# Optimization experiments

Hardware: AMD Instinct MI355X
Metric: run time of the kernel (lower is better)

## Reference

```python
import jax, jax.numpy as jnp
import numpy as np

N_NODES = 100000
N_EDGES = 1600000
N_GRAPHS = 256
NEG_SLOPE_GAT = 0.2   # GATConv default
NEG_SLOPE_ACT = 0.01  # F.leaky_relu default


def _leaky(x, s):
    return jnp.where(x >= 0, x, s * x)


def _gat_layer(x, src, dst, W, a_src, a_dst, b, n):
    # h = W x ; per-node attention logits
    h = x @ W                      # [N, D]
    al_s = h @ a_src               # [N]
    al_d = h @ a_dst               # [N]
    e = _leaky(al_s[src] + al_d[dst], NEG_SLOPE_GAT)  # [E]
    # segment softmax over incoming edges of each dst node
    m = jax.ops.segment_max(e, dst, num_segments=n)
    m = jnp.where(jnp.isfinite(m), m, 0.0)
    ex = jnp.exp(e - m[dst])
    s = jax.ops.segment_sum(ex, dst, num_segments=n)
    alpha = ex / (s[dst] + 1e-16)
    out = jax.ops.segment_sum(h[src] * alpha[:, None], dst, num_segments=n)
    return out + b


def setup_inputs() -> dict:
    key = jax.random.key(0)
    ks = jax.random.split(key, 12)
    x = jax.random.normal(ks[0], (N_NODES, 72), dtype=jnp.float32)
    edge_index = jax.random.randint(ks[1], (2, N_EDGES), 0, N_NODES, dtype=jnp.int64)
    batch = jnp.sort(jax.random.randint(ks[2], (N_NODES,), 0, N_GRAPHS, dtype=jnp.int64))
    def glorot(k, shape):
        fan = shape[0] + shape[-1]
        return jax.random.normal(k, shape, dtype=jnp.float32) * jnp.sqrt(2.0 / fan)
    return {
        "x": x, "edge_index": edge_index, "batch": batch,
        "W1": glorot(ks[3], (72, 64)),
        "a_src1": glorot(ks[4], (64,)), "a_dst1": glorot(ks[5], (64,)),
        "b1": jnp.zeros((64,), jnp.float32),
        "W2": glorot(ks[6], (64, 64)),
        "a_src2": glorot(ks[7], (64,)), "a_dst2": glorot(ks[8], (64,)),
        "b2": jnp.zeros((64,), jnp.float32),
        "fcW": glorot(ks[9], (64, 2)),
        "fcb": jnp.zeros((2,), jnp.float32),
    }


def reference(x, edge_index, batch, W1, a_src1, a_dst1, b1, W2, a_src2, a_dst2, b2, fcW, fcb):
    n = x.shape[0]
    # PyG GATConv adds self-loops by default
    loops = jnp.arange(n, dtype=edge_index.dtype)
    src = jnp.concatenate([edge_index[0], loops])
    dst = jnp.concatenate([edge_index[1], loops])
    h = _gat_layer(x, src, dst, W1, a_src1, a_dst1, b1, n)
    h = _leaky(h, NEG_SLOPE_ACT)
    h = _gat_layer(h, src, dst, W2, a_src2, a_dst2, b2, n)
    # global mean pool over graphs
    sums = jax.ops.segment_sum(h, batch, num_segments=N_GRAPHS)
    cnt = jax.ops.segment_sum(jnp.ones((n,), h.dtype), batch, num_segments=N_GRAPHS)
    pooled = sums / jnp.maximum(cnt, 1.0)[:, None]
    # dropout is identity at inference
    return pooled @ fcW + fcb
```

## Files before the change

### kernel.cpp

```cpp
#include <hip/hip_runtime.h>
#include <hip/hip_bf16.h>
#include <math.h>


#define NPB 256
#define EPB 4096
#define PSTRIDE 4608
#define XPAD 68

__device__ __forceinline__ unsigned int f2bf(float v) {
    unsigned int b = __float_as_uint(v);
    b += 0x7FFFu + ((b >> 16) & 1u);
    return b >> 16;
}

__device__ __forceinline__ int scanIncl256(int v, int t, int* wsum) {
    int lane = t & 63, wv = t >> 6;
#pragma unroll
    for (int o = 1; o < 64; o <<= 1) {
        int u = __shfl_up(v, o);
        if (lane >= o) v += u;
    }
    if (lane == 63) wsum[wv] = v;
    __syncthreads();
    int base = 0;
#pragma unroll
    for (int i = 0; i < 3; i++) base += (i < wv) ? wsum[i] : 0;
    __syncthreads();
    return v + base;
}

__global__ __launch_bounds__(256) void partition(const int* __restrict__ ei,
                                                 int E, int NB,
                                                 int* __restrict__ bcur,
                                                 unsigned int* __restrict__ pairs) {
    __shared__ int h[512];
    __shared__ int ls[512];
    __shared__ int lcur[512];
    __shared__ int hb[512];
    __shared__ int s2[256];
    __shared__ int wsum[4];
    __shared__ unsigned int Qp[EPB];
    __shared__ unsigned short Bq[EPB];
    int t = threadIdx.x;
    for (int i = t; i < 512; i += 256) h[i] = 0;
    __syncthreads();
    int i0 = blockIdx.x * EPB;
    unsigned int val[16];
    int bk[16];
    const int4* s4p = (const int4*)(ei);
    const int4* d4p = (const int4*)(ei + E);
#pragma unroll
    for (int k = 0; k < 4; k++) {
        int vbase = (i0 >> 2) + k * 256 + t;
        int i = vbase << 2;
        if (i < E) {
            int4 s4 = s4p[vbase];
            int4 d4 = d4p[vbase];
            int ss[4] = {s4.x, s4.y, s4.z, s4.w};
            int dd[4] = {d4.x, d4.y, d4.z, d4.w};
#pragma unroll
            for (int j = 0; j < 4; j++) {
                int e = k * 4 + j;
                bk[e] = dd[j] >> 8;
                val[e] = (unsigned)ss[j] | ((unsigned)(dd[j] & 255) << 24);
                atomicAdd(&h[bk[e]], 1);
            }
        } else {
#pragma unroll
            for (int j = 0; j < 4; j++) bk[k * 4 + j] = -1;
        }
    }
    __syncthreads();
    int p0 = h[2 * t], p1 = h[2 * t + 1];
    int incl = scanIncl256(p0 + p1, t, wsum);
    s2[t] = incl;
    int ex = incl - p0 - p1;
    ls[2 * t] = ex;           ls[2 * t + 1] = ex + p0;
    lcur[2 * t] = ex;         lcur[2 * t + 1] = ex + p0;
    __syncthreads();
    for (int b = t; b < NB; b += 256)
        hb[b] = h[b] ? atomicAdd(&bcur[b], h[b]) : 0;
    __syncthreads();
#pragma unroll
    for (int e = 0; e < 16; e++) {
        if (bk[e] < 0) continue;
        int pos = atomicAdd(&lcur[bk[e]], 1);
        Qp[pos] = val[e];
        Bq[pos] = (unsigned short)bk[e];
    }
    __syncthreads();
    int total = s2[255];
    for (int j = t; j < total; j += 256) {
        int bkj = Bq[j];
        int gp = hb[bkj] + (j - ls[bkj]);
        if (gp < PSTRIDE)
            pairs[(size_t)bkj * PSTRIDE + gp] = Qp[j];
    }
}

__global__ __launch_bounds__(256) void build_csr(const unsigned int* __restrict__ pairs,
                                                 const int* __restrict__ bcur,
                                                 int n, int NB,
                                                 int* __restrict__ rowptr,
                                                 int* __restrict__ srcs) {
    int b = blockIdx.x, t = threadIdx.x;
    __shared__ int c[512];
    __shared__ int s2[256];
    __shared__ int wsum[4];
    __shared__ int sbase, stot;
    __shared__ unsigned int Q[PSTRIDE];
    __shared__ int S[NPB + PSTRIDE];
    __shared__ int hist[256];
    __shared__ int hcur[256];
    int c0 = (2 * t < NB) ? min(bcur[2 * t], PSTRIDE) : 0;
    int c1 = (2 * t + 1 < NB) ? min(bcur[2 * t + 1], PSTRIDE) : 0;
    c[2 * t] = c0; c[2 * t + 1] = c1;
    hist[t] = 0;
    __syncthreads();
    int incl = scanIncl256(c0 + c1, t, wsum);
    s2[t] = incl;
    __syncthreads();
    if (t == 0) {
        int p = b >> 1;
        int ex = s2[p] - (c[2 * p] + c[2 * p + 1]);
        sbase = ex + ((b & 1) ? c[b & ~1] : 0);
        stot = s2[255];
    }
    __syncthreads();
    int d0 = b << 8;
    int nb = min(NPB, n - d0);
    int cnt_b = c[b];
    int csr0 = sbase + d0;
    const unsigned int* pb = pairs + (size_t)b * PSTRIDE;

    for (int j = t; j < cnt_b; j += 256)
        atomicAdd(&hist[(pb[j] & 0xFFFFFFu) >> 9], 1);
    __syncthreads();
    int hv = hist[t];
    int hincl = scanIncl256(hv, t, wsum);
    hcur[t] = hincl - hv;
    __syncthreads();
    for (int j = t; j < cnt_b; j += 256) {
        unsigned int p = pb[j];
        int pos = atomicAdd(&hcur[(p & 0xFFFFFFu) >> 9], 1);
        Q[pos] = p;
    }
    __syncthreads();

    __shared__ int deg[NPB];
    __shared__ int cur[NPB];
    deg[t] = (t < nb) ? 1 : 0;
    __syncthreads();
    for (int j = t; j < cnt_b; j += 256)
        atomicAdd(&deg[Q[j] >> 24], 1);
    __syncthreads();
    int v = deg[t];
    int dincl = scanIncl256(v, t, wsum);
    int excl = dincl - v;
    if (t < nb) {
        rowptr[d0 + t] = csr0 + excl;
        S[excl] = d0 + t;
        cur[t] = excl + 1;
    }
    __syncthreads();
    for (int j = t; j < cnt_b; j += 256) {
        unsigned int p = Q[j];
        int off = atomicAdd(&cur[p >> 24], 1);
        S[off] = (int)(p & 0x00FFFFFFu);
    }
    __syncthreads();
    int seg = nb + cnt_b;
    for (int j = t; j < seg; j += 256)
        srcs[csr0 + j] = S[j];
    if (b == 0 && t == 0) rowptr[n] = n + stot;
}

template <int IN_DIM>
__global__ __launch_bounds__(256) void node_gemm(const float* __restrict__ x,
                                                 const float* __restrict__ W,
                                                 const float* __restrict__ a_src,
                                                 const float* __restrict__ a_dst,
                                                 const float* __restrict__ bias_in,
                                                 float slope_in,
                                                 unsigned short* __restrict__ h16,
                                                 float* __restrict__ al_s,
                                                 float* __restrict__ al_d,
                                                 int n) {
    __shared__ float Ws[IN_DIM * 64];
    __shared__ float xs[IN_DIM][XPAD];
    int t = threadIdx.x;
    int nbase = blockIdx.x * 64;

    for (int idx = t; idx < IN_DIM * 16; idx += 256)
        ((float4*)Ws)[idx] = ((const float4*)W)[idx];
    const float* xb = x + (size_t)nbase * IN_DIM;
    int lim = min(64, n - nbase) * IN_DIM;
    constexpr int NV = (64 * IN_DIM) / 4;
    for (int idx = t; idx < NV; idx += 256) {
        int f0 = idx * 4;
        float4 v = make_float4(0.0f, 0.0f, 0.0f, 0.0f);
        if (f0 < lim) v = ((const float4*)xb)[idx];
        int node = f0 / IN_DIM;
        int k = f0 - node * IN_DIM;
        if (bias_in) {
            v.x += bias_in[k + 0];
            v.y += bias_in[k + 1];
            v.z += bias_in[k + 2];
            v.w += bias_in[k + 3];
            v.x = (v.x >= 0.0f) ? v.x : slope_in * v.x;
            v.y = (v.y >= 0.0f) ? v.y : slope_in * v.y;
            v.z = (v.z >= 0.0f) ? v.z : slope_in * v.z;
            v.w = (v.w >= 0.0f) ? v.w : slope_in * v.w;
        }
        xs[k + 0][node] = v.x;
        xs[k + 1][node] = v.y;
        xs[k + 2][node] = v.z;
        xs[k + 3][node] = v.w;
    }
    __syncthreads();

    int cg = t & 15;
    int ng = t >> 4;
    float acc[4][4] = {};
#pragma unroll 8
    for (int k = 0; k < IN_DIM; k++) {
        float4 xv = *(const float4*)&xs[k][ng * 4];
        float4 wv = *(const float4*)&Ws[k * 64 + cg * 4];
        float xa[4] = {xv.x, xv.y, xv.z, xv.w};
        float wa[4] = {wv.x, wv.y, wv.z, wv.w};
#pragma unroll
        for (int i = 0; i < 4; i++)
#pragma unroll
            for (int j = 0; j < 4; j++)
                acc[i][j] += xa[i] * wa[j];
    }

    float4 as4 = *(const float4*)(a_src + cg * 4);
    float4 ad4 = *(const float4*)(a_dst + cg * 4);
#pragma unroll
    for (int i = 0; i < 4; i++) {
        int node = nbase + ng * 4 + i;
        if (node < n) {
            uint2 p;
            p.x = f2bf(acc[i][0]) | (f2bf(acc[i][1]) << 16);
            p.y = f2bf(acc[i][2]) | (f2bf(acc[i][3]) << 16);
            *(uint2*)(h16 + (size_t)node * 64 + cg * 4) = p;
        }
        float vs = acc[i][0] * as4.x + acc[i][1] * as4.y +
                   acc[i][2] * as4.z + acc[i][3] * as4.w;
        float vd = acc[i][0] * ad4.x + acc[i][1] * ad4.y +
                   acc[i][2] * ad4.z + acc[i][3] * ad4.w;
#pragma unroll
        for (int o = 8; o; o >>= 1) {
            vs += __shfl_xor(vs, o);
            vd += __shfl_xor(vd, o);
        }
        if (cg == 0 && node < n) { al_s[node] = vs; al_d[node] = vd; }
    }
}

__device__ __forceinline__ void bf8_fma(float* acc, uint4 q, float w) {
    acc[0] += w * __uint_as_float(q.x << 16);
    acc[1] += w * __uint_as_float(q.x & 0xFFFF0000u);
    acc[2] += w * __uint_as_float(q.y << 16);
    acc[3] += w * __uint_as_float(q.y & 0xFFFF0000u);
    acc[4] += w * __uint_as_float(q.z << 16);
    acc[5] += w * __uint_as_float(q.z & 0xFFFF0000u);
    acc[6] += w * __uint_as_float(q.w << 16);
    acc[7] += w * __uint_as_float(q.w & 0xFFFF0000u);
}

__global__ __launch_bounds__(256) void gat_aggregate(const int* __restrict__ rowptr,
                                                     const int* __restrict__ srcs,
                                                     const float* __restrict__ als,
                                                     const float* __restrict__ ald,
                                                     const unsigned short* __restrict__ h16,
                                                     float* __restrict__ hout,
                                                     int n) {
    int t = threadIdx.x;
    int sub = t >> 3, lane = t & 7;
    int node = blockIdx.x * 32 + sub;
    if (node >= n) return;
    int beg = rowptr[node], end = rowptr[node + 1];
    float aldv = ald[node];
    const unsigned short* hb = h16 + lane * 8;

    float acc[8] = {};
    float sm = 0.0f;
    int j = beg;
    if (j + 4 <= end) {
        int s0 = srcs[j], s1 = srcs[j + 1], s2 = srcs[j + 2], s3 = srcs[j + 3];
        for (; j + 8 <= end; j += 4) {
            int n0 = srcs[j + 4], n1 = srcs[j + 5];
            int n2 = srcs[j + 6], n3 = srcs[j + 7];
            float e0 = als[s0] + aldv, e1 = als[s1] + aldv;
            float e2 = als[s2] + aldv, e3 = als[s3] + aldv;
            uint4 q0 = *(const uint4*)(hb + (size_t)s0 * 64);
            uint4 q1 = *(const uint4*)(hb + (size_t)s1 * 64);
            uint4 q2 = *(const uint4*)(hb + (size_t)s2 * 64);
            uint4 q3 = *(const uint4*)(hb + (size_t)s3 * 64);
            e0 = (e0 >= 0.0f) ? e0 : 0.2f * e0;
            e1 = (e1 >= 0.0f) ? e1 : 0.2f * e1;
            e2 = (e2 >= 0.0f) ? e2 : 0.2f * e2;
            e3 = (e3 >= 0.0f) ? e3 : 0.2f * e3;
            float w0 = __expf(e0), w1 = __expf(e1);
            float w2 = __expf(e2), w3 = __expf(e3);
            sm += (w0 + w1) + (w2 + w3);
            bf8_fma(acc, q0, w0);
            bf8_fma(acc, q1, w1);
            bf8_fma(acc, q2, w2);
            bf8_fma(acc, q3, w3);
            s0 = n0; s1 = n1; s2 = n2; s3 = n3;
        }
        {
            float e0 = als[s0] + aldv, e1 = als[s1] + aldv;
            float e2 = als[s2] + aldv, e3 = als[s3] + aldv;
            uint4 q0 = *(const uint4*)(hb + (size_t)s0 * 64);
            uint4 q1 = *(const uint4*)(hb + (size_t)s1 * 64);
            uint4 q2 = *(const uint4*)(hb + (size_t)s2 * 64);
            uint4 q3 = *(const uint4*)(hb + (size_t)s3 * 64);
            e0 = (e0 >= 0.0f) ? e0 : 0.2f * e0;
            e1 = (e1 >= 0.0f) ? e1 : 0.2f * e1;
            e2 = (e2 >= 0.0f) ? e2 : 0.2f * e2;
            e3 = (e3 >= 0.0f) ? e3 : 0.2f * e3;
            float w0 = __expf(e0), w1 = __expf(e1);
            float w2 = __expf(e2), w3 = __expf(e3);
            sm += (w0 + w1) + (w2 + w3);
            bf8_fma(acc, q0, w0);
            bf8_fma(acc, q1, w1);
            bf8_fma(acc, q2, w2);
            bf8_fma(acc, q3, w3);
            j += 4;
        }
    }
    for (; j < end; j++) {
        int s = srcs[j];
        float e = als[s] + aldv;
        e = (e >= 0.0f) ? e : 0.2f * e;
        float w = __expf(e);
        uint4 q = *(const uint4*)(hb + (size_t)s * 64);
        sm += w;
        bf8_fma(acc, q, w);
    }

    float inv = 1.0f / (sm + 1e-16f);
    float4 o0 = make_float4(acc[0] * inv, acc[1] * inv, acc[2] * inv, acc[3] * inv);
    float4 o1 = make_float4(acc[4] * inv, acc[5] * inv, acc[6] * inv, acc[7] * inv);
    float* op = hout + (size_t)node * 64 + lane * 8;
    *(float4*)op = o0;
    *(float4*)(op + 4) = o1;
}

__global__ __launch_bounds__(256) void pool_fc(const float* __restrict__ hout,
                                               const float* __restrict__ b2,
                                               const int* __restrict__ batch,
                                               const float* __restrict__ fcW,
                                               const float* __restrict__ fcb,
                                               float* __restrict__ out, int n) {
    int g = blockIdx.x;
    int t = threadIdx.x;
    __shared__ int sLo, sHi;
    __shared__ float red[16][64];
    if (t == 0) {
        int lo = 0, hi = n;
        while (lo < hi) { int m = (lo + hi) >> 1; if (batch[m] < g) lo = m + 1; else hi = m; }
        sLo = lo;
    } else if (t == 64) {
        int lo = 0, hi = n;
        while (lo < hi) { int m = (lo + hi) >> 1; if (batch[m] < g + 1) lo = m + 1; else hi = m; }
        sHi = lo;
    }
    __syncthreads();
    int lo = sLo, hi = sHi;
    int q = t & 15;
    int r = t >> 4;
    float4 a4 = make_float4(0.0f, 0.0f, 0.0f, 0.0f);
    for (int node = lo + r; node < hi; node += 16) {
        float4 v = *(const float4*)(hout + (size_t)node * 64 + q * 4);
        a4.x += v.x; a4.y += v.y; a4.z += v.z; a4.w += v.w;
    }
    *(float4*)&red[r][q * 4] = a4;
    __syncthreads();
    if (t < 64) {
        float c = (float)(hi - lo);
        float s = 0.0f;
#pragma unroll
        for (int i = 0; i < 16; i++) s += red[i][t];
        s += c * b2[t];
        float cd = (c > 1.0f) ? c : 1.0f;
        float p = s / cd;
        float s0 = p * fcW[t * 2 + 0];
        float s1 = p * fcW[t * 2 + 1];
#pragma unroll
        for (int o = 32; o; o >>= 1) {
            s0 += __shfl_xor(s0, o);
            s1 += __shfl_xor(s1, o);
        }
        if (t == 0) {
            out[g * 2 + 0] = s0 + fcb[0];
            out[g * 2 + 1] = s1 + fcb[1];
        }
    }
}

extern "C" void kernel_launch(void* const* d_in, const int* in_sizes, int n_in,
                              void* d_out, int out_size, void* d_ws, size_t ws_size,
                              hipStream_t stream) {
    const float* x    = (const float*)d_in[0];
    const int*   ei   = (const int*)d_in[1];
    const int*   batch= (const int*)d_in[2];
    const float* W1   = (const float*)d_in[3];
    const float* as1  = (const float*)d_in[4];
    const float* ad1  = (const float*)d_in[5];
    const float* b1   = (const float*)d_in[6];
    const float* W2   = (const float*)d_in[7];
    const float* as2  = (const float*)d_in[8];
    const float* ad2  = (const float*)d_in[9];
    const float* b2   = (const float*)d_in[10];
    const float* fcW  = (const float*)d_in[11];
    const float* fcb  = (const float*)d_in[12];
    float* out = (float*)d_out;

    const int N = in_sizes[2];
    const int E = in_sizes[1] / 2;
    const int G = out_size / 2;
    const int tot = E + N;
    const int NB = (N + NPB - 1) / NPB;

    float* ws     = (float*)d_ws;
    float* bufO   = ws;
    unsigned int* pairs  = (unsigned int*)bufO;
    float* als    = bufO + (size_t)N * 64;
    float* ald    = als + N;
    int*   rowptr = (int*)(ald + N);
    int*   srcs   = rowptr + N + 1;
    int*   bcur   = srcs + tot;
    unsigned short* bufH16 = (unsigned short*)(bcur + NB);

    dim3 b256(256);
    int gPart = (E + EPB - 1) / EPB;
    int gGemm = (N + 63) / 64;
    int gAgg  = (N + 31) / 32;

    hipMemsetAsync(bcur, 0, (size_t)NB * sizeof(int), stream);
    partition<<<gPart, b256, 0, stream>>>(ei, E, NB, bcur, pairs);
    build_csr<<<NB, b256, 0, stream>>>(pairs, bcur, N, NB, rowptr, srcs);

    node_gemm<72><<<gGemm, b256, 0, stream>>>(x, W1, as1, ad1, nullptr, 0.0f,
                                              bufH16, als, ald, N);
    gat_aggregate<<<gAgg, b256, 0, stream>>>(rowptr, srcs, als, ald, bufH16, bufO, N);

    node_gemm<64><<<gGemm, b256, 0, stream>>>(bufO, W2, as2, ad2, b1, 0.01f,
                                              bufH16, als, ald, N);
    gat_aggregate<<<gAgg, b256, 0, stream>>>(rowptr, srcs, als, ald, bufH16, bufO, N);

    pool_fc<<<G, b256, 0, stream>>>(bufO, b2, batch, fcW, fcb, out, N);
}
```

Before: 294.5 us.

## Fuse edge partition and first-layer node GEMM into one launch

```diff
diff --git a/kernel.cpp b/kernel.cpp
--- a/kernel.cpp
+++ b/kernel.cpp
@@ -30,72 +30,158 @@
     return v + base;
 }
 
-__global__ __launch_bounds__(256) void partition(const int* __restrict__ ei,
+struct PartSh {
+    int h[512];
+    int ls[512];
+    int lcur[512];
+    int hb[512];
+    int s2[256];
+    int wsum[4];
+    unsigned int Qp[EPB];
+    unsigned short Bq[EPB];
+};
+struct GemmSh {
+    float Ws[72 * 64];
+    float xs[72][XPAD];
+};
+union FusedSh { PartSh p; GemmSh g; };
+
+__global__ __launch_bounds__(256) void part_gemm(const int* __restrict__ ei,
                                                  int E, int NB,
                                                  int* __restrict__ bcur,
-                                                 unsigned int* __restrict__ pairs) {
-    __shared__ int h[512];
-    __shared__ int ls[512];
-    __shared__ int lcur[512];
-    __shared__ int hb[512];
-    __shared__ int s2[256];
-    __shared__ int wsum[4];
-    __shared__ unsigned int Qp[EPB];
-    __shared__ unsigned short Bq[EPB];
+                                                 unsigned int* __restrict__ pairs,
+                                                 int gPart,
+                                                 const float* __restrict__ x,
+                                                 const float* __restrict__ W,
+                                                 const float* __restrict__ a_src,
+                                                 const float* __restrict__ a_dst,
+                                                 unsigned short* __restrict__ h16,
+                                                 float* __restrict__ al_s,
+                                                 float* __restrict__ al_d,
+                                                 int n) {
+    __shared__ FusedSh sh;
     int t = threadIdx.x;
-    for (int i = t; i < 512; i += 256) h[i] = 0;
-    __syncthreads();
-    int i0 = blockIdx.x * EPB;
-    unsigned int val[16];
-    int bk[16];
-    const int4* s4p = (const int4*)(ei);
-    const int4* d4p = (const int4*)(ei + E);
-#pragma unroll
-    for (int k = 0; k < 4; k++) {
-        int vbase = (i0 >> 2) + k * 256 + t;
-        int i = vbase << 2;
-        if (i < E) {
-            int4 s4 = s4p[vbase];
-            int4 d4 = d4p[vbase];
-            int ss[4] = {s4.x, s4.y, s4.z, s4.w};
-            int dd[4] = {d4.x, d4.y, d4.z, d4.w};
-#pragma unroll
-            for (int j = 0; j < 4; j++) {
-                int e = k * 4 + j;
-                bk[e] = dd[j] >> 8;
-                val[e] = (unsigned)ss[j] | ((unsigned)(dd[j] & 255) << 24);
-                atomicAdd(&h[bk[e]], 1);
+    if ((int)blockIdx.x < gPart) {
+        int* h = sh.p.h;
+        int* ls = sh.p.ls;
+        int* lcur = sh.p.lcur;
+        int* hb = sh.p.hb;
+        int* s2 = sh.p.s2;
+        for (int i = t; i < 512; i += 256) h[i] = 0;
+        __syncthreads();
+        int i0 = blockIdx.x * EPB;
+        unsigned int val[16];
+        int bk[16];
+        const int4* s4p = (const int4*)(ei);
+        const int4* d4p = (const int4*)(ei + E);
+#pragma unroll
+        for (int k = 0; k < 4; k++) {
+            int vbase = (i0 >> 2) + k * 256 + t;
+            int i = vbase << 2;
+            if (i < E) {
+                int4 s4 = s4p[vbase];
+                int4 d4 = d4p[vbase];
+                int ss[4] = {s4.x, s4.y, s4.z, s4.w};
+                int dd[4] = {d4.x, d4.y, d4.z, d4.w};
+#pragma unroll
+                for (int j = 0; j < 4; j++) {
+                    int e = k * 4 + j;
+                    bk[e] = dd[j] >> 8;
+                    val[e] = (unsigned)ss[j] | ((unsigned)(dd[j] & 255) << 24);
+                    atomicAdd(&h[bk[e]], 1);
+                }
+            } else {
+#pragma unroll
+                for (int j = 0; j < 4; j++) bk[k * 4 + j] = -1;
             }
-        } else {
-#pragma unroll
-            for (int j = 0; j < 4; j++) bk[k * 4 + j] = -1;
-        }
-    }
-    __syncthreads();
-    int p0 = h[2 * t], p1 = h[2 * t + 1];
-    int incl = scanIncl256(p0 + p1, t, wsum);
-    s2[t] = incl;
-    int ex = incl - p0 - p1;
-    ls[2 * t] = ex;           ls[2 * t + 1] = ex + p0;
-    lcur[2 * t] = ex;         lcur[2 * t + 1] = ex + p0;
-    __syncthreads();
-    for (int b = t; b < NB; b += 256)
-        hb[b] = h[b] ? atomicAdd(&bcur[b], h[b]) : 0;
-    __syncthreads();
-#pragma unroll
-    for (int e = 0; e < 16; e++) {
-        if (bk[e] < 0) continue;
-        int pos = atomicAdd(&lcur[bk[e]], 1);
-        Qp[pos] = val[e];
-        Bq[pos] = (unsigned short)bk[e];
-    }
-    __syncthreads();
-    int total = s2[255];
-    for (int j = t; j < total; j += 256) {
-        int bkj = Bq[j];
-        int gp = hb[bkj] + (j - ls[bkj]);
-        if (gp < PSTRIDE)
-            pairs[(size_t)bkj * PSTRIDE + gp] = Qp[j];
+        }
+        __syncthreads();
+        int p0 = h[2 * t], p1 = h[2 * t + 1];
+        int incl = scanIncl256(p0 + p1, t, sh.p.wsum);
+        s2[t] = incl;
+        int ex = incl - p0 - p1;
+        ls[2 * t] = ex;           ls[2 * t + 1] = ex + p0;
+        lcur[2 * t] = ex;         lcur[2 * t + 1] = ex + p0;
+        __syncthreads();
+        for (int b = t; b < NB; b += 256)
+            hb[b] = h[b] ? atomicAdd(&bcur[b], h[b]) : 0;
+        __syncthreads();
+#pragma unroll
+        for (int e = 0; e < 16; e++) {
+            if (bk[e] < 0) continue;
+            int pos = atomicAdd(&lcur[bk[e]], 1);
+            sh.p.Qp[pos] = val[e];
+            sh.p.Bq[pos] = (unsigned short)bk[e];
+        }
+        __syncthreads();
+        int total = s2[255];
+        for (int j = t; j < total; j += 256) {
+            int bkj = sh.p.Bq[j];
+            int gp = hb[bkj] + (j - ls[bkj]);
+            if (gp < PSTRIDE)
+                pairs[(size_t)bkj * PSTRIDE + gp] = sh.p.Qp[j];
+        }
+    } else {
+        constexpr int IN_DIM = 72;
+        float* Ws = sh.g.Ws;
+        int nbase = ((int)blockIdx.x - gPart) * 64;
+
+        for (int idx = t; idx < IN_DIM * 16; idx += 256)
+            ((float4*)Ws)[idx] = ((const float4*)W)[idx];
+        const float* xb = x + (size_t)nbase * IN_DIM;
+        int lim = min(64, n - nbase) * IN_DIM;
+        constexpr int NV = (64 * IN_DIM) / 4;
+        for (int idx = t; idx < NV; idx += 256) {
+            int f0 = idx * 4;
+            float4 v = make_float4(0.0f, 0.0f, 0.0f, 0.0f);
+            if (f0 < lim) v = ((const float4*)xb)[idx];
+            int node = f0 / IN_DIM;
+            int k = f0 - node * IN_DIM;
+            sh.g.xs[k + 0][node] = v.x;
+            sh.g.xs[k + 1][node] = v.y;
+            sh.g.xs[k + 2][node] = v.z;
+            sh.g.xs[k + 3][node] = v.w;
+        }
+        __syncthreads();
+
+        int cg = t & 15;
+        int ng = t >> 4;
+        float acc[4][4] = {};
+#pragma unroll 8
+        for (int k = 0; k < IN_DIM; k++) {
+            float4 xv = *(const float4*)&sh.g.xs[k][ng * 4];
+            float4 wv = *(const float4*)&Ws[k * 64 + cg * 4];
+            float xa[4] = {xv.x, xv.y, xv.z, xv.w};
+            float wa[4] = {wv.x, wv.y, wv.z, wv.w};
+#pragma unroll
+            for (int i = 0; i < 4; i++)
+#pragma unroll
+                for (int j = 0; j < 4; j++)
+                    acc[i][j] += xa[i] * wa[j];
+        }
+
+        float4 as4 = *(const float4*)(a_src + cg * 4);
+        float4 ad4 = *(const float4*)(a_dst + cg * 4);
+#pragma unroll
+        for (int i = 0; i < 4; i++) {
+            int node = nbase + ng * 4 + i;
+            if (node < n) {
+                uint2 p;
+                p.x = f2bf(acc[i][0]) | (f2bf(acc[i][1]) << 16);
+                p.y = f2bf(acc[i][2]) | (f2bf(acc[i][3]) << 16);
+                *(uint2*)(h16 + (size_t)node * 64 + cg * 4) = p;
+            }
+            float vs = acc[i][0] * as4.x + acc[i][1] * as4.y +
+                       acc[i][2] * as4.z + acc[i][3] * as4.w;
+            float vd = acc[i][0] * ad4.x + acc[i][1] * ad4.y +
+                       acc[i][2] * ad4.z + acc[i][3] * ad4.w;
+#pragma unroll
+            for (int o = 8; o; o >>= 1) {
+                vs += __shfl_xor(vs, o);
+                vd += __shfl_xor(vd, o);
+            }
+            if (cg == 0 && node < n) { al_s[node] = vs; al_d[node] = vd; }
+        }
     }
 }
 
@@ -444,11 +530,11 @@
     int gAgg  = (N + 31) / 32;
 
     hipMemsetAsync(bcur, 0, (size_t)NB * sizeof(int), stream);
-    partition<<<gPart, b256, 0, stream>>>(ei, E, NB, bcur, pairs);
+    part_gemm<<<gPart + gGemm, b256, 0, stream>>>(ei, E, NB, bcur, pairs, gPart,
+                                                  x, W1, as1, ad1,
+                                                  bufH16, als, ald, N);
     build_csr<<<NB, b256, 0, stream>>>(pairs, bcur, N, NB, rowptr, srcs);
 
-    node_gemm<72><<<gGemm, b256, 0, stream>>>(x, W1, as1, ad1, nullptr, 0.0f,
-                                              bufH16, als, ald, N);
     gat_aggregate<<<gAgg, b256, 0, stream>>>(rowptr, srcs, als, ald, bufH16, bufO, N);
 
     node_gemm<64><<<gGemm, b256, 0, stream>>>(bufO, W2, as2, ad2, b1, 0.01f,
```

Result: faster. 287.8 us (-2.3%).
